# Optimization experiments

Hardware: AMD Instinct MI355X
Metric: run time of the kernel (lower is better)

The kernel has to match this reference:

```python
import jax, jax.numpy as jnp
import numpy as np

# irreps_in  = 128x0 + 64x1   (128 scalars, 64 vectors) -> dim 320
# irreps_out = 128x0 + 64x1 ; irreps_with_gates = (128+64)x0 + 64x1
B = 8192          # batch (nodes)
N0, N1 = 128, 64  # input multiplicities: scalars, vectors
NS, NV = 128, 64  # output scalars, gated vectors (NV gates appended to scalars)

_eps = np.zeros((3, 3, 3), np.float32)
_eps[0, 1, 2] = _eps[1, 2, 0] = _eps[2, 0, 1] = 1.0
_eps[0, 2, 1] = _eps[2, 1, 0] = _eps[1, 0, 2] = -1.0
EPS = jnp.asarray(_eps)  # Levi-Civita, used for the 1x1->1 CG path


def setup_inputs() -> dict:
    key = jax.random.key(0)
    ks = jax.random.split(key, 5)
    x = jax.random.normal(ks[0], (B, N0 + 3 * N1), jnp.float32)
    # fully-connected (uvw) path weights of the tensor square
    w000 = jax.random.normal(ks[1], (N0, N0, NS + NV), jnp.float32)
    w110 = jax.random.normal(ks[2], (N1, N1, NS + NV), jnp.float32)
    w011 = jax.random.normal(ks[3], (N0, N1, NV), jnp.float32)
    w111 = jax.random.normal(ks[4], (N1, N1, NV), jnp.float32)
    return {"x": x, "w000": w000, "w110": w110, "w011": w011, "w111": w111}


def reference(x, w000, w110, w011, w111):
    x0 = x[:, :N0]                        # [B, N0] scalars
    x1 = x[:, N0:].reshape(-1, N1, 3)     # [B, N1, 3] vectors

    inv_sqrt2 = 1.0 / np.sqrt(2.0)

    # ---- tensor square, scalar (l=0) outputs: NS scalars + NV gates ----
    s000 = jnp.einsum('bu,bv,uvw->bw', x0, x0, w000) * (1.0 / N0)
    dots = jnp.einsum('bui,bvi->buv', x1, x1) * (1.0 / np.sqrt(3.0))
    s110 = jnp.einsum('buv,uvw->bw', dots, w110) * (1.0 / N1)
    scalars = (s000 + s110) * inv_sqrt2   # [B, NS+NV], avg over 2 paths

    # ---- tensor square, vector (l=1) outputs: NV vectors ----
    v011 = jnp.einsum('bu,bvi,uvw->bwi', x0, x1, w011) * (1.0 / np.sqrt(N0 * N1))
    v111 = jnp.einsum('ijk,bui,bvj,uvw->bwk', EPS, x1, x1, w111) * (inv_sqrt2 / N1)
    vecs = (v011 + v111) * inv_sqrt2      # [B, NV, 3]

    # ---- e3nn.nn.Gate ----
    s_out = jax.nn.silu(scalars[:, :NS])            # act_scalars on true scalars
    g = jax.nn.sigmoid(scalars[:, NS:])             # act_gates on NV gate scalars
    v_out = vecs * g[:, :, None]                    # gate the non-scalar irreps

    return jnp.concatenate([s_out, v_out.reshape(v_out.shape[0], -1)], axis=1)
```

## Files before the change

kernel.cpp:

```cpp
#include <hip/hip_runtime.h>
#include <cstdint>

static constexpr int B_  = 8192;
static constexpr int NW_ = 192;

typedef __attribute__((ext_vector_type(8))) _Float16 h8v;
typedef __attribute__((ext_vector_type(2))) _Float16 h2v;
typedef __attribute__((ext_vector_type(4))) float f4v;
typedef __attribute__((ext_vector_type(2))) float f2v;
typedef __attribute__((ext_vector_type(4))) unsigned u4v;

#define DI __device__ __forceinline__

DI h2v uh(unsigned u) { return __builtin_bit_cast(h2v, u); }
DI unsigned hu(h2v h) { return __builtin_bit_cast(unsigned, h); }
DI h2v hsplat(unsigned short bits) {
  _Float16 v = __builtin_bit_cast(_Float16, bits);
  h2v t; t.x = v; t.y = v; return t;
}
DI unsigned hpack(float lo, float hi) {
  h2v t; t.x = (_Float16)lo; t.y = (_Float16)hi;
  return __builtin_bit_cast(unsigned, t);
}
DI short f2h_bits(float f) { return __builtin_bit_cast(short, (_Float16)f); }

DI f4v mfma16h(h8v a, h8v b, f4v c) {
  return __builtin_amdgcn_mfma_f32_16x16x32_f16(a, b, c, 0, 0, 0);
}

static constexpr unsigned PK_BU0 = 606436u;
static constexpr unsigned PK_BV0 = 1030628u;
static constexpr unsigned PK_BU2 = 4u;
static constexpr unsigned PK_BV2 = 20u;
DI int tab2(unsigned pack, int blk) { return (int)((pack >> (2 * blk)) & 3u); }

DI void prep_wsc_body(int g, const float* __restrict__ w000,
                      const float* __restrict__ w110, short* __restrict__ wf) {
  int lane = g & 63;
  int rest = g >> 6;
  int F = rest % 12;
  int s = rest / 12;
  int n = F * 16 + (lane & 15);
  int kk0 = (lane >> 4) << 3;
  const float s000 = 1.0f / (128.0f * 1.41421356237f);
  const float s110 = 1.0f / (64.0f * 2.44948974968f);
  short o[8];
  if (s < 320) {
    int blk = s >> 5, ik = s & 31;
    int bu = tab2(PK_BU0, blk), bv = tab2(PK_BV0, blk);
    int u = bu * 32 + ik;
#pragma unroll
    for (int j = 0; j < 8; ++j) {
      int v = bv * 32 + kk0 + j;
      float val = w000[(size_t)(u * 128 + v) * NW_ + n];
      if (bu != bv) val += w000[(size_t)(v * 128 + u) * NW_ + n];
      o[j] = f2h_bits(val * s000);
    }
  } else {
    int sp = s - 320;
    int blk = sp >> 5, ik = sp & 31;
    int bu = tab2(PK_BU2, blk), bv = tab2(PK_BV2, blk);
    int u = bu * 32 + ik;
#pragma unroll
    for (int j = 0; j < 8; ++j) {
      int v = bv * 32 + kk0 + j;
      float val = w110[(size_t)(u * 64 + v) * NW_ + n];
      if (bu != bv) val += w110[(size_t)(v * 64 + u) * NW_ + n];
      o[j] = f2h_bits(val * s110);
    }
  }
  *(h8v*)(wf + ((size_t)s * 12 + F) * 512 + lane * 8) = *(h8v*)o;
}

DI void prep_wvec_body(int g, const float* __restrict__ w011,
                       const float* __restrict__ w111, short* __restrict__ wf) {
  int lane = g & 63;
  int nf = (g >> 6) & 3;
  int s = g >> 8;
  int n = nf * 16 + (lane & 15);
  int kk0 = (lane >> 4) << 3;
  const float sv = 1.0f / 128.0f;
  short o[8];
  if (s < 256) {
#pragma unroll
    for (int j = 0; j < 8; ++j) {
      int k = s * 32 + kk0 + j;
      o[j] = f2h_bits(w011[(size_t)k * 64 + n] * sv);
    }
  } else {
    int sp = s - 256;
    int blk = sp >> 5, ik = sp & 31;
    int bu = tab2(PK_BU2, blk), bv = tab2(PK_BV2, blk);
    int u = bu * 32 + ik;
#pragma unroll
    for (int j = 0; j < 8; ++j) {
      int v = bv * 32 + kk0 + j;
      float val = w111[(size_t)(u * 64 + v) * 64 + n];
      if (bu != bv) val -= w111[(size_t)(v * 64 + u) * 64 + n];
      o[j] = f2h_bits(val * sv);
    }
  }
  *(h8v*)(wf + ((size_t)s * 4 + nf) * 512 + lane * 8) = *(h8v*)o;
}

__global__ void prep_all(const float* __restrict__ w000, const float* __restrict__ w110,
                         const float* __restrict__ w011, const float* __restrict__ w111,
                         short* __restrict__ wsc, short* __restrict__ wve) {
  if (blockIdx.x < 1248) {
    prep_wsc_body(blockIdx.x * 256 + threadIdx.x, w000, w110, wsc);
  } else {
    prep_wvec_body((blockIdx.x - 1248) * 256 + threadIdx.x, w011, w111, wve);
  }
}

#define X0H_STRIDE 136
#define X1_STRIDE  200

DI void stage_x32(const float* __restrict__ x, int b0,
                  unsigned short* X0H, unsigned short* X1) {
  const int t = threadIdx.x;
  const int row = t >> 3, l8 = t & 7;
  const float* src = x + (size_t)(b0 + row) * 320;
  unsigned o[8];
#pragma unroll
  for (int j = 0; j < 4; ++j) {
    f4v v = *(const f4v*)(src + l8 * 16 + j * 4);
    o[2 * j]     = hpack(v.x, v.y);
    o[2 * j + 1] = hpack(v.z, v.w);
  }
  *(u4v*)(&X0H[row * X0H_STRIDE + l8 * 16])     = u4v{o[0], o[1], o[2], o[3]};
  *(u4v*)(&X0H[row * X0H_STRIDE + l8 * 16 + 8]) = u4v{o[4], o[5], o[6], o[7]};
  float buf[24];
#pragma unroll
  for (int j = 0; j < 12; ++j) {
    f2v v = *(const f2v*)(src + 128 + l8 * 24 + j * 2);
    buf[2 * j] = v.x; buf[2 * j + 1] = v.y;
  }
#pragma unroll
  for (int i = 0; i < 3; ++i) {
    u4v w;
#pragma unroll
    for (int e = 0; e < 4; ++e)
      w[e] = hpack(buf[(2 * e) * 3 + i], buf[(2 * e + 1) * 3 + i]);
    *(u4v*)(&X1[row * X1_STRIDE + i * 64 + l8 * 8]) = w;
  }
}

DI void loadB6(h8v* dst, const short* __restrict__ p) {
#pragma unroll
  for (int nf = 0; nf < 6; ++nf) dst[nf] = *(const h8v*)(p + nf * 512);
}
DI void loadB2(h8v* dst, const short* __restrict__ p) {
  dst[0] = *(const h8v*)p;
  dst[1] = *(const h8v*)(p + 512);
}

__global__ __launch_bounds__(256, 2)
void gemm_fused(const float* __restrict__ x, const short* __restrict__ wsc,
                const short* __restrict__ wve,
                float* __restrict__ acc_sc, float* __restrict__ acc_ve) {
  __shared__ unsigned short X0H[32 * X0H_STRIDE];
  __shared__ unsigned short X1[32 * X1_STRIDE];
  __shared__ f4v dump[2][12][64];
  const int xcd = blockIdx.x & 7;
  const int wi  = blockIdx.x >> 3;
  const int path = wi & 1;
  const int tile = xcd * 32 + (wi >> 1);
  const int b0 = tile * 32;

  stage_x32(x, b0, X0H, X1);
  __syncthreads();

  const int t0 = threadIdx.x;
  const int w = t0 >> 6, lane = t0 & 63;
  const int nh = w & 1, kh = w >> 1;
  const int q = lane >> 4, r = lane & 15, q8 = q * 8;

  if (path == 0) {
    const unsigned short* x0f[2];
    const unsigned short* x1f[2];
#pragma unroll
    for (int f = 0; f < 2; ++f) {
      x0f[f] = &X0H[(f * 16 + r) * X0H_STRIDE];
      x1f[f] = &X1[(f * 16 + r) * X1_STRIDE];
    }

    f4v acc[2][6];
#pragma unroll
    for (int f = 0; f < 2; ++f)
#pragma unroll
      for (int nf = 0; nf < 6; ++nf) acc[f][nf] = f4v{0.f, 0.f, 0.f, 0.f};

    {
      const int s0 = kh * 160;
      const short* wp = wsc + ((size_t)s0 * 12 + nh * 6) * 512 + lane * 8;
      u4v pv[2];
#pragma unroll
      for (int f = 0; f < 2; ++f) pv[f] = u4v{0, 0, 0, 0};
      int bu32 = 0;
      h8v ba[6], bb[6];
      loadB6(ba, wp);
      auto step = [&](int t, const h8v* b) {
        const int s = s0 + t;
        const int ik = s & 31;
        if (t == 0 || ik == 0) {
          const int blk = s >> 5;
          const int bv32 = tab2(PK_BV0, blk) * 32;
          bu32 = tab2(PK_BU0, blk) * 32;
#pragma unroll
          for (int f = 0; f < 2; ++f) pv[f] = *(const u4v*)(x0f[f] + bv32 + q8);
        }
        h8v a[2];
#pragma unroll
        for (int f = 0; f < 2; ++f) {
          h2v xu = hsplat(x0f[f][bu32 + ik]);
          u4v pa;
#pragma unroll
          for (int m = 0; m < 4; ++m) pa[m] = hu(uh(pv[f][m]) * xu);
          a[f] = __builtin_bit_cast(h8v, pa);
        }
        __builtin_amdgcn_s_setprio(1);
#pragma unroll
        for (int nf = 0; nf < 6; ++nf)
#pragma unroll
          for (int f = 0; f < 2; ++f)
            acc[f][nf] = mfma16h(a[f], b[nf], acc[f][nf]);
        __builtin_amdgcn_s_setprio(0);
      };
      for (int t2 = 0; t2 < 80; ++t2) {
        loadB6(bb, wp + 6144);
        step(2 * t2, ba);
        if (t2 != 79) loadB6(ba, wp + 12288);
        step(2 * t2 + 1, bb);
        wp += 12288;
      }
    }

    {
      const int sp0 = kh * 48;
      const short* wp = wsc + ((size_t)(320 + sp0) * 12 + nh * 6) * 512 + lane * 8;
      h8v ba[6], bb[6];
      loadB6(ba, wp);
      auto step = [&](int t, const h8v* b) {
        const int sp = sp0 + t;
        const int blk = sp >> 5, ik = sp & 31;
        const int bu32 = tab2(PK_BU2, blk) * 32;
        const int bv32 = tab2(PK_BV2, blk) * 32;
        h8v a[2];
#pragma unroll
        for (int f = 0; f < 2; ++f) {
          h2v us0 = hsplat(x1f[f][bu32 + ik]);
          h2v us1 = hsplat(x1f[f][64 + bu32 + ik]);
          h2v us2 = hsplat(x1f[f][128 + bu32 + ik]);
          u4v p0 = *(const u4v*)(x1f[f] + bv32 + q8);
          u4v p1 = *(const u4v*)(x1f[f] + 64 + bv32 + q8);
          u4v p2 = *(const u4v*)(x1f[f] + 128 + bv32 + q8);
          u4v pa;
#pragma unroll
          for (int m = 0; m < 4; ++m) {
            h2v sm = uh(p0[m]) * us0;
            sm = sm + uh(p1[m]) * us1;
            sm = sm + uh(p2[m]) * us2;
            pa[m] = hu(sm);
          }
          a[f] = __builtin_bit_cast(h8v, pa);
        }
        __builtin_amdgcn_s_setprio(1);
#pragma unroll
        for (int nf = 0; nf < 6; ++nf)
#pragma unroll
          for (int f = 0; f < 2; ++f)
            acc[f][nf] = mfma16h(a[f], b[nf], acc[f][nf]);
        __builtin_amdgcn_s_setprio(0);
      };
      for (int t2 = 0; t2 < 24; ++t2) {
        loadB6(bb, wp + 6144);
        step(2 * t2, ba);
        if (t2 != 23) loadB6(ba, wp + 12288);
        step(2 * t2 + 1, bb);
        wp += 12288;
      }
    }

    if (kh == 1) {
#pragma unroll
      for (int f = 0; f < 2; ++f)
#pragma unroll
        for (int nf = 0; nf < 6; ++nf)
          dump[nh][f * 6 + nf][lane] = acc[f][nf];
    }
    __syncthreads();
    if (kh == 0) {
#pragma unroll
      for (int f = 0; f < 2; ++f)
#pragma unroll
        for (int nf = 0; nf < 6; ++nf) {
          f4v v = acc[f][nf] + dump[nh][f * 6 + nf][lane];
          int n = (nh * 6 + nf) * 16 + r;
#pragma unroll
          for (int reg = 0; reg < 4; ++reg) {
            int rowo = b0 + f * 16 + q * 4 + reg;
            acc_sc[(size_t)rowo * NW_ + n] = v[reg];
          }
        }
    }
  } else {
    const unsigned short* x0r[2];
    const unsigned short* x1r[2];
#pragma unroll
    for (int ff = 0; ff < 2; ++ff) {
      x0r[ff] = &X0H[(ff * 16 + r) * X0H_STRIDE];
      x1r[ff] = &X1[(ff * 16 + r) * X1_STRIDE];
    }

    f4v acc[2][3][2];
#pragma unroll
    for (int ff = 0; ff < 2; ++ff)
#pragma unroll
      for (int ip = 0; ip < 3; ++ip)
#pragma unroll
        for (int nfl = 0; nfl < 2; ++nfl) acc[ff][ip][nfl] = f4v{0.f, 0.f, 0.f, 0.f};

    {
      const int u0 = kh * 64;
      const short* wp = wve + (size_t)(u0 * 2) * 2048 + nh * 1024 + lane * 8;
      h8v ba[2], bb[2];
      loadB2(ba, wp);
      auto vstep = [&](int st, const h8v* b) {
        const int g = st >> 1, j = st & 1;
        const int vb = j * 32 + q8;
        h8v a[2][3];
#pragma unroll
        for (int ff = 0; ff < 2; ++ff) {
          h2v xu2 = hsplat(x0r[ff][u0 + g]);
#pragma unroll
          for (int i = 0; i < 3; ++i) {
            u4v p = *(const u4v*)(x1r[ff] + i * 64 + vb);
            u4v pa;
#pragma unroll
            for (int m = 0; m < 4; ++m) pa[m] = hu(uh(p[m]) * xu2);
            a[ff][i] = __builtin_bit_cast(h8v, pa);
          }
        }
        __builtin_amdgcn_s_setprio(1);
#pragma unroll
        for (int ip = 0; ip < 3; ++ip)
#pragma unroll
          for (int nfl = 0; nfl < 2; ++nfl)
#pragma unroll
            for (int ff = 0; ff < 2; ++ff)
              acc[ff][ip][nfl] = mfma16h(a[ff][ip], b[nfl], acc[ff][ip][nfl]);
        __builtin_amdgcn_s_setprio(0);
      };
      for (int t2 = 0; t2 < 64; ++t2) {
        loadB2(bb, wp + 2048);
        vstep(2 * t2, ba);
        if (t2 != 63) loadB2(ba, wp + 4096);
        vstep(2 * t2 + 1, bb);
        wp += 4096;
      }
    }

    {
      const int sp0 = kh * 48;
      const short* wp = wve + (size_t)(256 + sp0) * 2048 + nh * 1024 + lane * 8;
      h8v ba[2], bb[2];
      loadB2(ba, wp);
      auto vstep = [&](int t, const h8v* b) {
        const int sp = sp0 + t;
        const int blk = sp >> 5, ik = sp & 31;
        const int bu32 = tab2(PK_BU2, blk) * 32;
        const int bv32 = tab2(PK_BV2, blk) * 32;
        h8v a[2][3];
#pragma unroll
        for (int ff = 0; ff < 2; ++ff) {
          h2v us[3];
          u4v p[3];
#pragma unroll
          for (int i = 0; i < 3; ++i) {
            us[i] = hsplat(x1r[ff][i * 64 + bu32 + ik]);
            p[i] = *(const u4v*)(x1r[ff] + i * 64 + bv32 + q8);
          }
#pragma unroll
          for (int ip = 0; ip < 3; ++ip) {
            const int i1 = (ip + 1) % 3, i2 = (ip + 2) % 3;
            u4v pa;
#pragma unroll
            for (int m = 0; m < 4; ++m)
              pa[m] = hu(uh(p[i2][m]) * us[i1] - uh(p[i1][m]) * us[i2]);
            a[ff][ip] = __builtin_bit_cast(h8v, pa);
          }
        }
        __builtin_amdgcn_s_setprio(1);
#pragma unroll
        for (int ip = 0; ip < 3; ++ip)
#pragma unroll
          for (int nfl = 0; nfl < 2; ++nfl)
#pragma unroll
            for (int ff = 0; ff < 2; ++ff)
              acc[ff][ip][nfl] = mfma16h(a[ff][ip], b[nfl], acc[ff][ip][nfl]);
        __builtin_amdgcn_s_setprio(0);
      };
      for (int t2 = 0; t2 < 24; ++t2) {
        loadB2(bb, wp + 2048);
        vstep(2 * t2, ba);
        if (t2 != 23) loadB2(ba, wp + 4096);
        vstep(2 * t2 + 1, bb);
        wp += 4096;
      }
    }

    if (kh == 1) {
#pragma unroll
      for (int ff = 0; ff < 2; ++ff)
#pragma unroll
        for (int ip = 0; ip < 3; ++ip)
#pragma unroll
          for (int nfl = 0; nfl < 2; ++nfl)
            dump[nh][(ff * 3 + ip) * 2 + nfl][lane] = acc[ff][ip][nfl];
    }
    __syncthreads();
    if (kh == 0) {
#pragma unroll
      for (int ff = 0; ff < 2; ++ff)
#pragma unroll
        for (int ip = 0; ip < 3; ++ip)
#pragma unroll
          for (int nfl = 0; nfl < 2; ++nfl) {
            f4v v = acc[ff][ip][nfl] + dump[nh][(ff * 3 + ip) * 2 + nfl][lane];
            int n = (nh * 2 + nfl) * 16 + r;
#pragma unroll
            for (int reg = 0; reg < 4; ++reg) {
              int rowo = ip * B_ + b0 + ff * 16 + q * 4 + reg;
              acc_ve[(size_t)rowo * 64 + n] = v[reg];
            }
          }
    }
  }
}

__global__ void epilogue(const float* __restrict__ sc, const float* __restrict__ ve,
                         float* __restrict__ out) {
  int t = blockIdx.x * blockDim.x + threadIdx.x;
  int b = t / NW_, c = t % NW_;
  float v = sc[t];
  float sg = 1.0f / (1.0f + __expf(-v));
  if (c < 128) {
    out[(size_t)b * 320 + c] = v * sg;
  } else {
    int w = c - 128;
#pragma unroll
    for (int i = 0; i < 3; ++i) {
      float vv = ve[((size_t)i * B_ + b) * 64 + w];
      out[(size_t)b * 320 + 128 + w * 3 + i] = vv * sg;
    }
  }
}

extern "C" void kernel_launch(void* const* d_in, const int* in_sizes, int n_in,
                              void* d_out, int out_size, void* d_ws, size_t ws_size,
                              hipStream_t stream) {
  const float* x    = (const float*)d_in[0];
  const float* w000 = (const float*)d_in[1];
  const float* w110 = (const float*)d_in[2];
  const float* w011 = (const float*)d_in[3];
  const float* w111 = (const float*)d_in[4];
  float* out = (float*)d_out;

  char* ws = (char*)d_ws;
  float* acc_sc = (float*)ws;
  float* acc_ve = (float*)(ws + 6291456);
  short* wsc    = (short*)(ws + 12582912);
  short* wve    = (short*)(ws + 17694720);

  prep_all  <<<1600, 256, 0, stream>>>(w000, w110, w011, w111, wsc, wve);
  gemm_fused<<<512, 256, 0, stream>>>(x, wsc, wve, acc_sc, acc_ve);
  epilogue  <<<6144, 256, 0, stream>>>(acc_sc, acc_ve, out);
}
```

Baseline: 178.8 us.

## Fuse gate epilogue into GEMM, merge paths per block, coalesce weight prep

Merges the scalar and vector paths into one 512-thread block per 32-row tile, so the sigmoid gates are passed through shared memory and the final output is written directly. This removes the separate epilogue kernel and its fp32 accumulator round-trip through global memory. The weight-prep kernel is rewritten to read source weights with coalesced vector loads and transpose them through LDS. The B-fragment prefetch is deepened to a four-slot register ring. Risks include higher register pressure at 512 threads with two blocks per CU, only 256 blocks to fill the GPU, and the dropped XCD-aware tile mapping.

Result: faster. 159.0 us (-11.1%).

```diff
diff --git a/kernel.cpp b/kernel.cpp
--- a/kernel.cpp
+++ b/kernel.cpp
@@ -9,6 +9,7 @@
 typedef __attribute__((ext_vector_type(4))) float f4v;
 typedef __attribute__((ext_vector_type(2))) float f2v;
 typedef __attribute__((ext_vector_type(4))) unsigned u4v;
+typedef __attribute__((ext_vector_type(2))) unsigned u2v;
 
 #define DI __device__ __forceinline__
 
@@ -34,115 +35,128 @@
 static constexpr unsigned PK_BV2 = 20u;
 DI int tab2(unsigned pack, int blk) { return (int)((pack >> (2 * blk)) & 3u); }
 
-DI void prep_wsc_body(int g, const float* __restrict__ w000,
-                      const float* __restrict__ w110, short* __restrict__ wf) {
-  int lane = g & 63;
-  int rest = g >> 6;
-  int F = rest % 12;
-  int s = rest / 12;
-  int n = F * 16 + (lane & 15);
-  int kk0 = (lane >> 4) << 3;
-  const float s000 = 1.0f / (128.0f * 1.41421356237f);
-  const float s110 = 1.0f / (64.0f * 2.44948974968f);
-  short o[8];
-  if (s < 320) {
-    int blk = s >> 5, ik = s & 31;
-    int bu = tab2(PK_BU0, blk), bv = tab2(PK_BV0, blk);
-    int u = bu * 32 + ik;
-#pragma unroll
-    for (int j = 0; j < 8; ++j) {
-      int v = bv * 32 + kk0 + j;
-      float val = w000[(size_t)(u * 128 + v) * NW_ + n];
-      if (bu != bv) val += w000[(size_t)(v * 128 + u) * NW_ + n];
-      o[j] = f2h_bits(val * s000);
-    }
-  } else {
-    int sp = s - 320;
-    int blk = sp >> 5, ik = sp & 31;
-    int bu = tab2(PK_BU2, blk), bv = tab2(PK_BV2, blk);
-    int u = bu * 32 + ik;
-#pragma unroll
-    for (int j = 0; j < 8; ++j) {
-      int v = bv * 32 + kk0 + j;
-      float val = w110[(size_t)(u * 64 + v) * NW_ + n];
-      if (bu != bv) val += w110[(size_t)(v * 64 + u) * NW_ + n];
-      o[j] = f2h_bits(val * s110);
-    }
-  }
-  *(h8v*)(wf + ((size_t)s * 12 + F) * 512 + lane * 8) = *(h8v*)o;
-}
-
-DI void prep_wvec_body(int g, const float* __restrict__ w011,
-                       const float* __restrict__ w111, short* __restrict__ wf) {
-  int lane = g & 63;
-  int nf = (g >> 6) & 3;
-  int s = g >> 8;
-  int n = nf * 16 + (lane & 15);
-  int kk0 = (lane >> 4) << 3;
-  const float sv = 1.0f / 128.0f;
-  short o[8];
-  if (s < 256) {
-#pragma unroll
-    for (int j = 0; j < 8; ++j) {
-      int k = s * 32 + kk0 + j;
-      o[j] = f2h_bits(w011[(size_t)k * 64 + n] * sv);
-    }
-  } else {
-    int sp = s - 256;
-    int blk = sp >> 5, ik = sp & 31;
-    int bu = tab2(PK_BU2, blk), bv = tab2(PK_BV2, blk);
-    int u = bu * 32 + ik;
-#pragma unroll
-    for (int j = 0; j < 8; ++j) {
-      int v = bv * 32 + kk0 + j;
-      float val = w111[(size_t)(u * 64 + v) * 64 + n];
-      if (bu != bv) val -= w111[(size_t)(v * 64 + u) * 64 + n];
-      o[j] = f2h_bits(val * sv);
-    }
-  }
-  *(h8v*)(wf + ((size_t)s * 4 + nf) * 512 + lane * 8) = *(h8v*)o;
-}
-
 __global__ void prep_all(const float* __restrict__ w000, const float* __restrict__ w110,
                          const float* __restrict__ w011, const float* __restrict__ w111,
                          short* __restrict__ wsc, short* __restrict__ wve) {
-  if (blockIdx.x < 1248) {
-    prep_wsc_body(blockIdx.x * 256 + threadIdx.x, w000, w110, wsc);
+  __shared__ unsigned short T[32][200];
+  const int t = threadIdx.x;
+  const int bi = blockIdx.x;
+  const float s000 = 1.0f / (128.0f * 1.41421356237f);
+  const float s110 = 1.0f / (64.0f * 2.44948974968f);
+  const float sv   = 1.0f / 128.0f;
+
+  if (bi < 416) {
+    const int s = bi;
+    const float* W; int dim; float scale; int blk, ik, bu, bv;
+    if (s < 320) {
+      blk = s >> 5; ik = s & 31;
+      bu = tab2(PK_BU0, blk); bv = tab2(PK_BV0, blk);
+      W = w000; dim = 128; scale = s000;
+    } else {
+      int sp = s - 320; blk = sp >> 5; ik = sp & 31;
+      bu = tab2(PK_BU2, blk); bv = tab2(PK_BV2, blk);
+      W = w110; dim = 64; scale = s110;
+    }
+    const int u = bu * 32 + ik;
+    const int v = t >> 3, l8 = t & 7;
+    float a[24];
+    const float* pA = W + ((size_t)(u * dim) + bv * 32 + v) * 192 + l8 * 24;
+#pragma unroll
+    for (int jj = 0; jj < 6; ++jj) {
+      f4v x4 = *(const f4v*)(pA + jj * 4);
+      a[jj * 4] = x4.x; a[jj * 4 + 1] = x4.y; a[jj * 4 + 2] = x4.z; a[jj * 4 + 3] = x4.w;
+    }
+    if (bu != bv) {
+      const float* pB = W + ((size_t)((bv * 32 + v)) * dim + u) * 192 + l8 * 24;
+#pragma unroll
+      for (int jj = 0; jj < 6; ++jj) {
+        f4v x4 = *(const f4v*)(pB + jj * 4);
+        a[jj * 4] += x4.x; a[jj * 4 + 1] += x4.y; a[jj * 4 + 2] += x4.z; a[jj * 4 + 3] += x4.w;
+      }
+    }
+    unsigned o[12];
+#pragma unroll
+    for (int i = 0; i < 12; ++i) o[i] = hpack(a[2 * i] * scale, a[2 * i + 1] * scale);
+#pragma unroll
+    for (int i = 0; i < 3; ++i)
+      *(u4v*)(&T[v][l8 * 24 + i * 8]) = u4v{o[4 * i], o[4 * i + 1], o[4 * i + 2], o[4 * i + 3]};
+    __syncthreads();
+    short* dst = wsc + (size_t)s * 6144;
+#pragma unroll
+    for (int k = 0; k < 3; ++k) {
+      const int unit = t * 3 + k;
+      const int F = unit >> 6, lane = unit & 63;
+      const int n = F * 16 + (lane & 15);
+      const int vr = (lane >> 4) * 8;
+      short oo[8];
+#pragma unroll
+      for (int j = 0; j < 8; ++j) oo[j] = (short)T[vr + j][n];
+      *(h8v*)(dst + F * 512 + lane * 8) = *(h8v*)oo;
+    }
   } else {
-    prep_wvec_body((blockIdx.x - 1248) * 256 + threadIdx.x, w011, w111, wve);
+    const int s = bi - 416;
+    if (s < 256) {
+      const int k32 = t >> 3, l8 = t & 7;
+      const float* p = w011 + ((size_t)(s * 32 + k32)) * 64 + l8 * 8;
+      f4v x0_ = *(const f4v*)p, x1_ = *(const f4v*)(p + 4);
+      u4v o{hpack(x0_.x * sv, x0_.y * sv), hpack(x0_.z * sv, x0_.w * sv),
+            hpack(x1_.x * sv, x1_.y * sv), hpack(x1_.z * sv, x1_.w * sv)};
+      *(u4v*)(&T[k32][l8 * 8]) = o;
+    } else {
+      const int sp = s - 256;
+      const int blk = sp >> 5, ik = sp & 31;
+      const int bu = tab2(PK_BU2, blk), bv = tab2(PK_BV2, blk);
+      const int u = bu * 32 + ik;
+      const int v = t >> 3, l8 = t & 7;
+      float a[8];
+      const float* pA = w111 + ((size_t)(u * 64) + bv * 32 + v) * 64 + l8 * 8;
+      f4v x0_ = *(const f4v*)pA, x1_ = *(const f4v*)(pA + 4);
+      a[0] = x0_.x; a[1] = x0_.y; a[2] = x0_.z; a[3] = x0_.w;
+      a[4] = x1_.x; a[5] = x1_.y; a[6] = x1_.z; a[7] = x1_.w;
+      if (bu != bv) {
+        const float* pB = w111 + ((size_t)((bv * 32 + v)) * 64 + u) * 64 + l8 * 8;
+        f4v y0 = *(const f4v*)pB, y1 = *(const f4v*)(pB + 4);
+        a[0] -= y0.x; a[1] -= y0.y; a[2] -= y0.z; a[3] -= y0.w;
+        a[4] -= y1.x; a[5] -= y1.y; a[6] -= y1.z; a[7] -= y1.w;
+      }
+      u4v o{hpack(a[0] * sv, a[1] * sv), hpack(a[2] * sv, a[3] * sv),
+            hpack(a[4] * sv, a[5] * sv), hpack(a[6] * sv, a[7] * sv)};
+      *(u4v*)(&T[v][l8 * 8]) = o;
+    }
+    __syncthreads();
+    const int nf = t >> 6, lane = t & 63;
+    const int n = nf * 16 + (lane & 15);
+    const int vr = (lane >> 4) * 8;
+    short oo[8];
+#pragma unroll
+    for (int j = 0; j < 8; ++j) oo[j] = (short)T[vr + j][n];
+    *(h8v*)(wve + (size_t)s * 2048 + nf * 512 + lane * 8) = *(h8v*)oo;
   }
 }
 
 #define X0H_STRIDE 136
 #define X1_STRIDE  200
 
-DI void stage_x32(const float* __restrict__ x, int b0,
-                  unsigned short* X0H, unsigned short* X1) {
+DI void stage_x32w(const float* __restrict__ x, int b0,
+                   unsigned short* X0H, unsigned short* X1) {
   const int t = threadIdx.x;
-  const int row = t >> 3, l8 = t & 7;
+  const int row = t >> 4, l16 = t & 15;
   const float* src = x + (size_t)(b0 + row) * 320;
-  unsigned o[8];
-#pragma unroll
-  for (int j = 0; j < 4; ++j) {
-    f4v v = *(const f4v*)(src + l8 * 16 + j * 4);
-    o[2 * j]     = hpack(v.x, v.y);
-    o[2 * j + 1] = hpack(v.z, v.w);
-  }
-  *(u4v*)(&X0H[row * X0H_STRIDE + l8 * 16])     = u4v{o[0], o[1], o[2], o[3]};
-  *(u4v*)(&X0H[row * X0H_STRIDE + l8 * 16 + 8]) = u4v{o[4], o[5], o[6], o[7]};
-  float buf[24];
-#pragma unroll
-  for (int j = 0; j < 12; ++j) {
-    f2v v = *(const f2v*)(src + 128 + l8 * 24 + j * 2);
-    buf[2 * j] = v.x; buf[2 * j + 1] = v.y;
-  }
+  f4v v0 = *(const f4v*)(src + l16 * 8);
+  f4v v1 = *(const f4v*)(src + l16 * 8 + 4);
+  u4v o{hpack(v0.x, v0.y), hpack(v0.z, v0.w), hpack(v1.x, v1.y), hpack(v1.z, v1.w)};
+  *(u4v*)(&X0H[row * X0H_STRIDE + l16 * 8]) = o;
+  float buf[12];
+  f4v a0 = *(const f4v*)(src + 128 + l16 * 12);
+  f4v a1 = *(const f4v*)(src + 128 + l16 * 12 + 4);
+  f4v a2 = *(const f4v*)(src + 128 + l16 * 12 + 8);
+  buf[0] = a0.x; buf[1] = a0.y; buf[2] = a0.z; buf[3] = a0.w;
+  buf[4] = a1.x; buf[5] = a1.y; buf[6] = a1.z; buf[7] = a1.w;
+  buf[8] = a2.x; buf[9] = a2.y; buf[10] = a2.z; buf[11] = a2.w;
 #pragma unroll
   for (int i = 0; i < 3; ++i) {
-    u4v w;
-#pragma unroll
-    for (int e = 0; e < 4; ++e)
-      w[e] = hpack(buf[(2 * e) * 3 + i], buf[(2 * e + 1) * 3 + i]);
-    *(u4v*)(&X1[row * X1_STRIDE + i * 64 + l8 * 8]) = w;
+    u2v w2{hpack(buf[i], buf[3 + i]), hpack(buf[6 + i], buf[9 + i])};
+    *(u2v*)(&X1[row * X1_STRIDE + i * 64 + l16 * 4]) = w2;
   }
 }
 
@@ -155,28 +169,29 @@
   dst[1] = *(const h8v*)(p + 512);
 }
 
-__global__ __launch_bounds__(256, 2)
+__global__ __launch_bounds__(512, 2)
 void gemm_fused(const float* __restrict__ x, const short* __restrict__ wsc,
-                const short* __restrict__ wve,
-                float* __restrict__ acc_sc, float* __restrict__ acc_ve) {
+                const short* __restrict__ wve, float* __restrict__ out) {
   __shared__ unsigned short X0H[32 * X0H_STRIDE];
   __shared__ unsigned short X1[32 * X1_STRIDE];
-  __shared__ f4v dump[2][12][64];
-  const int xcd = blockIdx.x & 7;
-  const int wi  = blockIdx.x >> 3;
-  const int path = wi & 1;
-  const int tile = xcd * 32 + (wi >> 1);
-  const int b0 = tile * 32;
-
-  stage_x32(x, b0, X0H, X1);
+  __shared__ f4v dump[4][12][64];
+  __shared__ float G[32][64];
+  const int b0 = blockIdx.x * 32;
+
+  stage_x32w(x, b0, X0H, X1);
   __syncthreads();
 
   const int t0 = threadIdx.x;
   const int w = t0 >> 6, lane = t0 & 63;
-  const int nh = w & 1, kh = w >> 1;
+  const bool isvec = w >= 4;
+  const int nh = w & 1, kh = (w >> 1) & 1;
   const int q = lane >> 4, r = lane & 15, q8 = q * 8;
 
-  if (path == 0) {
+  f4v acc[12];
+#pragma unroll
+  for (int i = 0; i < 12; ++i) acc[i] = f4v{0.f, 0.f, 0.f, 0.f};
+
+  if (!isvec) {
     const unsigned short* x0f[2];
     const unsigned short* x1f[2];
 #pragma unroll
@@ -185,124 +200,89 @@
       x1f[f] = &X1[(f * 16 + r) * X1_STRIDE];
     }
 
-    f4v acc[2][6];
-#pragma unroll
-    for (int f = 0; f < 2; ++f)
-#pragma unroll
-      for (int nf = 0; nf < 6; ++nf) acc[f][nf] = f4v{0.f, 0.f, 0.f, 0.f};
-
     {
       const int s0 = kh * 160;
       const short* wp = wsc + ((size_t)s0 * 12 + nh * 6) * 512 + lane * 8;
-      u4v pv[2];
-#pragma unroll
-      for (int f = 0; f < 2; ++f) pv[f] = u4v{0, 0, 0, 0};
+      u4v pv[2]; pv[0] = u4v{0, 0, 0, 0}; pv[1] = u4v{0, 0, 0, 0};
       int bu32 = 0;
-      h8v ba[6], bb[6];
-      loadB6(ba, wp);
-      auto step = [&](int t, const h8v* b) {
-        const int s = s0 + t;
-        const int ik = s & 31;
-        if (t == 0 || ik == 0) {
-          const int blk = s >> 5;
-          const int bv32 = tab2(PK_BV0, blk) * 32;
-          bu32 = tab2(PK_BU0, blk) * 32;
-#pragma unroll
-          for (int f = 0; f < 2; ++f) pv[f] = *(const u4v*)(x0f[f] + bv32 + q8);
-        }
-        h8v a[2];
-#pragma unroll
-        for (int f = 0; f < 2; ++f) {
-          h2v xu = hsplat(x0f[f][bu32 + ik]);
-          u4v pa;
-#pragma unroll
-          for (int m = 0; m < 4; ++m) pa[m] = hu(uh(pv[f][m]) * xu);
-          a[f] = __builtin_bit_cast(h8v, pa);
-        }
-        __builtin_amdgcn_s_setprio(1);
-#pragma unroll
-        for (int nf = 0; nf < 6; ++nf)
-#pragma unroll
-          for (int f = 0; f < 2; ++f)
-            acc[f][nf] = mfma16h(a[f], b[nf], acc[f][nf]);
-        __builtin_amdgcn_s_setprio(0);
-      };
-      for (int t2 = 0; t2 < 80; ++t2) {
-        loadB6(bb, wp + 6144);
-        step(2 * t2, ba);
-        if (t2 != 79) loadB6(ba, wp + 12288);
-        step(2 * t2 + 1, bb);
-        wp += 12288;
+      h8v b[4][6];
+      loadB6(b[0], wp); loadB6(b[1], wp + 6144); loadB6(b[2], wp + 12288);
+      for (int t4 = 0; t4 < 40; ++t4) {
+#pragma unroll
+        for (int uu = 0; uu < 4; ++uu) {
+          const int t = t4 * 4 + uu;
+          if (t < 157) loadB6(b[(uu + 3) & 3], wp + (size_t)(t + 3) * 6144);
+          const int s = s0 + t;
+          const int ik = s & 31;
+          if (t == 0 || ik == 0) {
+            const int blk = s >> 5;
+            const int bv32 = tab2(PK_BV0, blk) * 32;
+            bu32 = tab2(PK_BU0, blk) * 32;
+            pv[0] = *(const u4v*)(x0f[0] + bv32 + q8);
+            pv[1] = *(const u4v*)(x0f[1] + bv32 + q8);
+          }
+          h8v a[2];
+#pragma unroll
+          for (int f = 0; f < 2; ++f) {
+            h2v xu = hsplat(x0f[f][bu32 + ik]);
+            u4v pa;
+#pragma unroll
+            for (int m = 0; m < 4; ++m) pa[m] = hu(uh(pv[f][m]) * xu);
+            a[f] = __builtin_bit_cast(h8v, pa);
+          }
+          __builtin_amdgcn_s_setprio(1);
+#pragma unroll
+          for (int nf = 0; nf < 6; ++nf)
+#pragma unroll
+            for (int f = 0; f < 2; ++f)
+              acc[f * 6 + nf] = mfma16h(a[f], b[uu & 3][nf], acc[f * 6 + nf]);
+          __builtin_amdgcn_s_setprio(0);
+        }
       }
     }
 
     {
       const int sp0 = kh * 48;
       const short* wp = wsc + ((size_t)(320 + sp0) * 12 + nh * 6) * 512 + lane * 8;
-      h8v ba[6], bb[6];
-      loadB6(ba, wp);
-      auto step = [&](int t, const h8v* b) {
-        const int sp = sp0 + t;
-        const int blk = sp >> 5, ik = sp & 31;
-        const int bu32 = tab2(PK_BU2, blk) * 32;
-        const int bv32 = tab2(PK_BV2, blk) * 32;
-        h8v a[2];
-#pragma unroll
-        for (int f = 0; f < 2; ++f) {
-          h2v us0 = hsplat(x1f[f][bu32 + ik]);
-          h2v us1 = hsplat(x1f[f][64 + bu32 + ik]);
-          h2v us2 = hsplat(x1f[f][128 + bu32 + ik]);
-          u4v p0 = *(const u4v*)(x1f[f] + bv32 + q8);
-          u4v p1 = *(const u4v*)(x1f[f] + 64 + bv32 + q8);
-          u4v p2 = *(const u4v*)(x1f[f] + 128 + bv32 + q8);
-          u4v pa;
-#pragma unroll
-          for (int m = 0; m < 4; ++m) {
-            h2v sm = uh(p0[m]) * us0;
-            sm = sm + uh(p1[m]) * us1;
-            sm = sm + uh(p2[m]) * us2;
-            pa[m] = hu(sm);
-          }
-          a[f] = __builtin_bit_cast(h8v, pa);
-        }
-        __builtin_amdgcn_s_setprio(1);
-#pragma unroll
-        for (int nf = 0; nf < 6; ++nf)
-#pragma unroll
-          for (int f = 0; f < 2; ++f)
-            acc[f][nf] = mfma16h(a[f], b[nf], acc[f][nf]);
-        __builtin_amdgcn_s_setprio(0);
-      };
-      for (int t2 = 0; t2 < 24; ++t2) {
-        loadB6(bb, wp + 6144);
-        step(2 * t2, ba);
-        if (t2 != 23) loadB6(ba, wp + 12288);
-        step(2 * t2 + 1, bb);
-        wp += 12288;
-      }
-    }
-
-    if (kh == 1) {
-#pragma unroll
-      for (int f = 0; f < 2; ++f)
-#pragma unroll
-        for (int nf = 0; nf < 6; ++nf)
-          dump[nh][f * 6 + nf][lane] = acc[f][nf];
-    }
-    __syncthreads();
-    if (kh == 0) {
-#pragma unroll
-      for (int f = 0; f < 2; ++f)
-#pragma unroll
-        for (int nf = 0; nf < 6; ++nf) {
-          f4v v = acc[f][nf] + dump[nh][f * 6 + nf][lane];
-          int n = (nh * 6 + nf) * 16 + r;
-#pragma unroll
-          for (int reg = 0; reg < 4; ++reg) {
-            int rowo = b0 + f * 16 + q * 4 + reg;
-            acc_sc[(size_t)rowo * NW_ + n] = v[reg];
-          }
-        }
+      h8v b[4][6];
+      loadB6(b[0], wp); loadB6(b[1], wp + 6144); loadB6(b[2], wp + 12288);
+      for (int t4 = 0; t4 < 12; ++t4) {
+#pragma unroll
+        for (int uu = 0; uu < 4; ++uu) {
+          const int t = t4 * 4 + uu;
+          if (t < 45) loadB6(b[(uu + 3) & 3], wp + (size_t)(t + 3) * 6144);
+          const int sp = sp0 + t;
+          const int blk = sp >> 5, ik = sp & 31;
+          const int bu32 = tab2(PK_BU2, blk) * 32;
+          const int bv32 = tab2(PK_BV2, blk) * 32;
+          h8v a[2];
+#pragma unroll
+          for (int f = 0; f < 2; ++f) {
+            h2v us0 = hsplat(x1f[f][bu32 + ik]);
+            h2v us1 = hsplat(x1f[f][64 + bu32 + ik]);
+            h2v us2 = hsplat(x1f[f][128 + bu32 + ik]);
+            u4v p0 = *(const u4v*)(x1f[f] + bv32 + q8);
+            u4v p1 = *(const u4v*)(x1f[f] + 64 + bv32 + q8);
+            u4v p2 = *(const u4v*)(x1f[f] + 128 + bv32 + q8);
+            u4v pa;
+#pragma unroll
+            for (int m = 0; m < 4; ++m) {
+              h2v sm = uh(p0[m]) * us0;
+              sm = sm + uh(p1[m]) * us1;
+              sm = sm + uh(p2[m]) * us2;
+              pa[m] = hu(sm);
+            }
+            a[f] = __builtin_bit_cast(h8v, pa);
+          }
+          __builtin_amdgcn_s_setprio(1);
+#pragma unroll
+          for (int nf = 0; nf < 6; ++nf)
+#pragma unroll
+            for (int f = 0; f < 2; ++f)
+              acc[f * 6 + nf] = mfma16h(a[f], b[uu & 3][nf], acc[f * 6 + nf]);
+          __builtin_amdgcn_s_setprio(0);
+        }
+      }
     }
   } else {
     const unsigned short* x0r[2];
@@ -313,147 +293,136 @@
       x1r[ff] = &X1[(ff * 16 + r) * X1_STRIDE];
     }
 
-    f4v acc[2][3][2];
-#pragma unroll
-    for (int ff = 0; ff < 2; ++ff)
-#pragma unroll
-      for (int ip = 0; ip < 3; ++ip)
-#pragma unroll
-        for (int nfl = 0; nfl < 2; ++nfl) acc[ff][ip][nfl] = f4v{0.f, 0.f, 0.f, 0.f};
-
     {
       const int u0 = kh * 64;
       const short* wp = wve + (size_t)(u0 * 2) * 2048 + nh * 1024 + lane * 8;
-      h8v ba[2], bb[2];
-      loadB2(ba, wp);
-      auto vstep = [&](int st, const h8v* b) {
-        const int g = st >> 1, j = st & 1;
-        const int vb = j * 32 + q8;
-        h8v a[2][3];
-#pragma unroll
-        for (int ff = 0; ff < 2; ++ff) {
-          h2v xu2 = hsplat(x0r[ff][u0 + g]);
-#pragma unroll
-          for (int i = 0; i < 3; ++i) {
-            u4v p = *(const u4v*)(x1r[ff] + i * 64 + vb);
-            u4v pa;
-#pragma unroll
-            for (int m = 0; m < 4; ++m) pa[m] = hu(uh(p[m]) * xu2);
-            a[ff][i] = __builtin_bit_cast(h8v, pa);
-          }
-        }
-        __builtin_amdgcn_s_setprio(1);
-#pragma unroll
-        for (int ip = 0; ip < 3; ++ip)
-#pragma unroll
-          for (int nfl = 0; nfl < 2; ++nfl)
-#pragma unroll
-            for (int ff = 0; ff < 2; ++ff)
-              acc[ff][ip][nfl] = mfma16h(a[ff][ip], b[nfl], acc[ff][ip][nfl]);
-        __builtin_amdgcn_s_setprio(0);
-      };
-      for (int t2 = 0; t2 < 64; ++t2) {
-        loadB2(bb, wp + 2048);
-        vstep(2 * t2, ba);
-        if (t2 != 63) loadB2(ba, wp + 4096);
-        vstep(2 * t2 + 1, bb);
-        wp += 4096;
+      h8v b[4][2];
+      loadB2(b[0], wp); loadB2(b[1], wp + 2048); loadB2(b[2], wp + 4096);
+      for (int t4 = 0; t4 < 32; ++t4) {
+#pragma unroll
+        for (int uu = 0; uu < 4; ++uu) {
+          const int t = t4 * 4 + uu;
+          if (t < 125) loadB2(b[(uu + 3) & 3], wp + (size_t)(t + 3) * 2048);
+          const int g = t >> 1, j = t & 1;
+          const int vb = j * 32 + q8;
+          h8v a[2][3];
+#pragma unroll
+          for (int ff = 0; ff < 2; ++ff) {
+            h2v xu2 = hsplat(x0r[ff][u0 + g]);
+#pragma unroll
+            for (int i = 0; i < 3; ++i) {
+              u4v p = *(const u4v*)(x1r[ff] + i * 64 + vb);
+              u4v pa;
+#pragma unroll
+              for (int m = 0; m < 4; ++m) pa[m] = hu(uh(p[m]) * xu2);
+              a[ff][i] = __builtin_bit_cast(h8v, pa);
+            }
+          }
+          __builtin_amdgcn_s_setprio(1);
+#pragma unroll
+          for (int ip = 0; ip < 3; ++ip)
+#pragma unroll
+            for (int nfl = 0; nfl < 2; ++nfl)
+#pragma unroll
+              for (int ff = 0; ff < 2; ++ff)
+                acc[(ff * 3 + ip) * 2 + nfl] =
+                    mfma16h(a[ff][ip], b[uu & 3][nfl], acc[(ff * 3 + ip) * 2 + nfl]);
+          __builtin_amdgcn_s_setprio(0);
+        }
       }
     }
 
     {
       const int sp0 = kh * 48;
       const short* wp = wve + (size_t)(256 + sp0) * 2048 + nh * 1024 + lane * 8;
-      h8v ba[2], bb[2];
-      loadB2(ba, wp);
-      auto vstep = [&](int t, const h8v* b) {
-        const int sp = sp0 + t;
-        const int blk = sp >> 5, ik = sp & 31;
-        const int bu32 = tab2(PK_BU2, blk) * 32;
-        const int bv32 = tab2(PK_BV2, blk) * 32;
-        h8v a[2][3];
-#pragma unroll
-        for (int ff = 0; ff < 2; ++ff) {
-          h2v us[3];
-          u4v p[3];
-#pragma unroll
-          for (int i = 0; i < 3; ++i) {
-            us[i] = hsplat(x1r[ff][i * 64 + bu32 + ik]);
-            p[i] = *(const u4v*)(x1r[ff] + i * 64 + bv32 + q8);
-          }
-#pragma unroll
-          for (int ip = 0; ip < 3; ++ip) {
-            const int i1 = (ip + 1) % 3, i2 = (ip + 2) % 3;
-            u4v pa;
-#pragma unroll
-            for (int m = 0; m < 4; ++m)
-              pa[m] = hu(uh(p[i2][m]) * us[i1] - uh(p[i1][m]) * us[i2]);
-            a[ff][ip] = __builtin_bit_cast(h8v, pa);
-          }
-        }
-        __builtin_amdgcn_s_setprio(1);
-#pragma unroll
-        for (int ip = 0; ip < 3; ++ip)
-#pragma unroll
-          for (int nfl = 0; nfl < 2; ++nfl)
-#pragma unroll
-            for (int ff = 0; ff < 2; ++ff)
-              acc[ff][ip][nfl] = mfma16h(a[ff][ip], b[nfl], acc[ff][ip][nfl]);
-        __builtin_amdgcn_s_setprio(0);
-      };
-      for (int t2 = 0; t2 < 24; ++t2) {
-        loadB2(bb, wp + 2048);
-        vstep(2 * t2, ba);
-        if (t2 != 23) loadB2(ba, wp + 4096);
-        vstep(2 * t2 + 1, bb);
-        wp += 4096;
-      }
-    }
-
-    if (kh == 1) {
-#pragma unroll
-      for (int ff = 0; ff < 2; ++ff)
-#pragma unroll
-        for (int ip = 0; ip < 3; ++ip)
-#pragma unroll
-          for (int nfl = 0; nfl < 2; ++nfl)
-            dump[nh][(ff * 3 + ip) * 2 + nfl][lane] = acc[ff][ip][nfl];
-    }
-    __syncthreads();
-    if (kh == 0) {
-#pragma unroll
-      for (int ff = 0; ff < 2; ++ff)
-#pragma unroll
-        for (int ip = 0; ip < 3; ++ip)
-#pragma unroll
-          for (int nfl = 0; nfl < 2; ++nfl) {
-            f4v v = acc[ff][ip][nfl] + dump[nh][(ff * 3 + ip) * 2 + nfl][lane];
-            int n = (nh * 2 + nfl) * 16 + r;
-#pragma unroll
-            for (int reg = 0; reg < 4; ++reg) {
-              int rowo = ip * B_ + b0 + ff * 16 + q * 4 + reg;
-              acc_ve[(size_t)rowo * 64 + n] = v[reg];
+      h8v b[4][2];
+      loadB2(b[0], wp); loadB2(b[1], wp + 2048); loadB2(b[2], wp + 4096);
+      for (int t4 = 0; t4 < 12; ++t4) {
+#pragma unroll
+        for (int uu = 0; uu < 4; ++uu) {
+          const int t = t4 * 4 + uu;
+          if (t < 45) loadB2(b[(uu + 3) & 3], wp + (size_t)(t + 3) * 2048);
+          const int sp = sp0 + t;
+          const int blk = sp >> 5, ik = sp & 31;
+          const int bu32 = tab2(PK_BU2, blk) * 32;
+          const int bv32 = tab2(PK_BV2, blk) * 32;
+          h8v a[2][3];
+#pragma unroll
+          for (int ff = 0; ff < 2; ++ff) {
+            h2v us[3];
+            u4v p[3];
+#pragma unroll
+            for (int i = 0; i < 3; ++i) {
+              us[i] = hsplat(x1r[ff][i * 64 + bu32 + ik]);
+              p[i] = *(const u4v*)(x1r[ff] + i * 64 + bv32 + q8);
             }
-          }
-    }
-  }
-}
-
-__global__ void epilogue(const float* __restrict__ sc, const float* __restrict__ ve,
-                         float* __restrict__ out) {
-  int t = blockIdx.x * blockDim.x + threadIdx.x;
-  int b = t / NW_, c = t % NW_;
-  float v = sc[t];
-  float sg = 1.0f / (1.0f + __expf(-v));
-  if (c < 128) {
-    out[(size_t)b * 320 + c] = v * sg;
-  } else {
-    int w = c - 128;
-#pragma unroll
-    for (int i = 0; i < 3; ++i) {
-      float vv = ve[((size_t)i * B_ + b) * 64 + w];
-      out[(size_t)b * 320 + 128 + w * 3 + i] = vv * sg;
-    }
+#pragma unroll
+            for (int ip = 0; ip < 3; ++ip) {
+              const int i1 = (ip + 1) % 3, i2 = (ip + 2) % 3;
+              u4v pa;
+#pragma unroll
+              for (int m = 0; m < 4; ++m)
+                pa[m] = hu(uh(p[i2][m]) * us[i1] - uh(p[i1][m]) * us[i2]);
+              a[ff][ip] = __builtin_bit_cast(h8v, pa);
+            }
+          }
+          __builtin_amdgcn_s_setprio(1);
+#pragma unroll
+          for (int ip = 0; ip < 3; ++ip)
+#pragma unroll
+            for (int nfl = 0; nfl < 2; ++nfl)
+#pragma unroll
+              for (int ff = 0; ff < 2; ++ff)
+                acc[(ff * 3 + ip) * 2 + nfl] =
+                    mfma16h(a[ff][ip], b[uu & 3][nfl], acc[(ff * 3 + ip) * 2 + nfl]);
+          __builtin_amdgcn_s_setprio(0);
+        }
+      }
+    }
+  }
+
+  const int slot = (isvec ? 2 : 0) + nh;
+  if (kh == 1) {
+#pragma unroll
+    for (int i = 0; i < 12; ++i) dump[slot][i][lane] = acc[i];
+  }
+  __syncthreads();
+
+  if (kh == 0 && !isvec) {
+#pragma unroll
+    for (int f = 0; f < 2; ++f)
+#pragma unroll
+      for (int nf = 0; nf < 6; ++nf) {
+        f4v v = acc[f * 6 + nf] + dump[slot][f * 6 + nf][lane];
+        const int n = (nh * 6 + nf) * 16 + r;
+#pragma unroll
+        for (int reg = 0; reg < 4; ++reg) {
+          const int row = f * 16 + q * 4 + reg;
+          const float val = v[reg];
+          const float sg = 1.0f / (1.0f + __expf(-val));
+          if (n < 128) out[(size_t)(b0 + row) * 320 + n] = val * sg;
+          else         G[row][n - 128] = sg;
+        }
+      }
+  }
+  __syncthreads();
+
+  if (kh == 0 && isvec) {
+#pragma unroll
+    for (int ff = 0; ff < 2; ++ff)
+#pragma unroll
+      for (int ip = 0; ip < 3; ++ip)
+#pragma unroll
+        for (int nfl = 0; nfl < 2; ++nfl) {
+          const int ai = (ff * 3 + ip) * 2 + nfl;
+          f4v v = acc[ai] + dump[slot][ai][lane];
+          const int n = (nh * 2 + nfl) * 16 + r;
+#pragma unroll
+          for (int reg = 0; reg < 4; ++reg) {
+            const int row = ff * 16 + q * 4 + reg;
+            out[(size_t)(b0 + row) * 320 + 128 + n * 3 + ip] = v[reg] * G[row][n];
+          }
+        }
   }
 }
 
@@ -468,12 +437,9 @@
   float* out = (float*)d_out;
 
   char* ws = (char*)d_ws;
-  float* acc_sc = (float*)ws;
-  float* acc_ve = (float*)(ws + 6291456);
-  short* wsc    = (short*)(ws + 12582912);
-  short* wve    = (short*)(ws + 17694720);
-
-  prep_all  <<<1600, 256, 0, stream>>>(w000, w110, w011, w111, wsc, wve);
-  gemm_fused<<<512, 256, 0, stream>>>(x, wsc, wve, acc_sc, acc_ve);
-  epilogue  <<<6144, 256, 0, stream>>>(acc_sc, acc_ve, out);
-}
+  short* wsc = (short*)ws;
+  short* wve = (short*)(ws + 5111808);
+
+  prep_all  <<<768, 256, 0, stream>>>(w000, w110, w011, w111, wsc, wve);
+  gemm_fused<<<256, 512, 0, stream>>>(x, wsc, wve, out);
+}
```
